# Performance work log

Hardware: AMD Instinct MI355X
Metric: run time of the kernel (lower is better)

Reference implementation:

```python
import jax, jax.numpy as jnp
import numpy as np

DIM = 128
WH, WW = 8, 8
N = WH * WW            # tokens per window = 64
H = 8                  # num_heads
HD = DIM // H          # head_dim = 16
SCALE = HD ** -0.5
B = 2                  # true batch
NW = 1024              # windows per image (256x256 / 8x8)
B_ = B * NW            # 2048 windows total
NFT = 2                # num_frame_type
TABLE = (2 * WH - 1) * (2 * WW - 1)  # 225


def _relative_position_index():
    coords = np.stack(np.meshgrid(np.arange(WH), np.arange(WW), indexing='ij'))  # (2, WH, WW)
    cf = coords.reshape(2, -1)                        # (2, N)
    rel = cf[:, :, None] - cf[:, None, :]             # (2, N, N)
    rel = rel.transpose(1, 2, 0).astype(np.int64)     # (N, N, 2)
    rel[..., 0] += WH - 1
    rel[..., 1] += WW - 1
    rel[..., 0] *= 2 * WW - 1
    return rel.sum(-1)                                # (N, N) in [0, 224]


def setup_inputs() -> dict:
    key = jax.random.key(0)
    ks = jax.random.split(key, 12)
    x = jax.random.normal(ks[0], (B_, N, DIM), dtype=jnp.float32)
    # 0 / -100 additive window mask (shifted-window pattern surrogate)
    mask = jnp.where(jax.random.uniform(ks[1], (NW, N, N)) > 0.9, -100.0, 0.0).astype(jnp.float32)
    frame_type = jax.random.uniform(ks[2], (B, NFT), dtype=jnp.float32)
    qkv_w = jax.random.normal(ks[3], (3 * DIM, DIM), dtype=jnp.float32) * 0.02
    qkv_b = jnp.zeros((3 * DIM,), dtype=jnp.float32)
    table = jax.random.normal(ks[4], (TABLE, H), dtype=jnp.float32) * 0.02
    proj_w = jax.random.normal(ks[5], (DIM, DIM), dtype=jnp.float32) * 0.02
    proj_b = jnp.zeros((DIM,), dtype=jnp.float32)
    aff_w1 = jax.random.normal(ks[6], (16, NFT), dtype=jnp.float32) * 0.1
    aff_b1 = jnp.zeros((16,), dtype=jnp.float32)
    aff_w2 = jax.random.normal(ks[7], (2 * DIM, 16), dtype=jnp.float32) * 0.1
    rel_index = jnp.asarray(_relative_position_index(), dtype=jnp.int32)
    return {"x": x, "mask": mask, "frame_type": frame_type,
            "qkv_w": qkv_w, "qkv_b": qkv_b, "table": table,
            "proj_w": proj_w, "proj_b": proj_b,
            "aff_w1": aff_w1, "aff_b1": aff_b1, "aff_w2": aff_w2,
            "rel_index": rel_index}


def reference(x, mask, frame_type, qkv_w, qkv_b, table, proj_w, proj_b,
              aff_w1, aff_b1, aff_w2, rel_index):
    # qkv projection: (B_, N, 3C) -> (3, B_, H, N, HD)
    qkv = (x @ qkv_w.T + qkv_b).reshape(B_, N, 3, H, HD).transpose(2, 0, 3, 1, 4)
    q, k, v = qkv[0], qkv[1], qkv[2]
    attn = jnp.einsum('bhnd,bhmd->bhnm', q * SCALE, k)          # (B_, H, N, N)
    rpb = table[rel_index].transpose(2, 0, 1)                    # (H, N, N)
    attn = attn + rpb[None]
    # add window mask: (B, NW, H, N, N)
    attn = attn.reshape(B_ // NW, NW, H, N, N) + mask[None, :, None]
    attn = jax.nn.softmax(attn.reshape(B_, H, N, N), axis=-1)
    # FA affine modulation of V
    hdn = jax.nn.sigmoid(frame_type @ aff_w1.T + aff_b1)         # (B, 16)
    ap = hdn @ aff_w2.T                                          # (B, 2C)
    scale_p, bias_p = jnp.split(ap, 2, axis=-1)                  # each (B, C)
    scale_p = jnp.repeat(scale_p, B_ // B, axis=0).reshape(B_, H, 1, HD)
    bias_p = jnp.repeat(bias_p, B_ // B, axis=0).reshape(B_, H, 1, HD)
    v = jax.nn.softplus(scale_p) * v + bias_p
    out = jnp.einsum('bhnm,bhmd->bhnd', attn, v)                 # (B_, H, N, HD)
    out = out.transpose(0, 2, 1, 3).reshape(B_, N, DIM)
    return out @ proj_w.T + proj_b
```

## Files before the change

### kernel.cpp

```cpp
#include <hip/hip_runtime.h>
#include <hip/hip_bf16.h>

#define NWIN 2048
#define OFF_AFF 0
#define OFF_RPB 512
#define OFF_WQ  33280
#define OFF_WP  82432

typedef __attribute__((ext_vector_type(8))) __bf16 bf16x8;
typedef __attribute__((ext_vector_type(4))) float floatx4;

__global__ __launch_bounds__(256) void prep_kernel(
    const float* __restrict__ frame_type, const float* __restrict__ qkv_w,
    const float* __restrict__ table, const float* __restrict__ proj_w,
    const float* __restrict__ aff_w1, const float* __restrict__ aff_b1,
    const float* __restrict__ aff_w2, const int* __restrict__ rel_index,
    float* __restrict__ ws)
{
  const int gid = blockIdx.x * 256 + threadIdx.x;
  if (gid < 98304) {
    int j = gid & 7, lane = (gid >> 3) & 63, kt = (gid >> 9) & 3, nt = gid >> 11;
    int n = nt * 16 + (lane & 15);
    int k = kt * 32 + (lane >> 4) * 8 + j;
    ((__bf16*)(ws + OFF_WQ))[gid] = (__bf16)qkv_w[n * 128 + k];
  }
  if (gid < 16384) {
    int j = gid & 7, lane = (gid >> 3) & 63, kt = (gid >> 9) & 3, nt = gid >> 11;
    int n = nt * 16 + (lane & 15);
    int k = kt * 32 + (lane >> 4) * 8 + j;
    ((__bf16*)(ws + OFF_WP))[gid] = (__bf16)proj_w[n * 128 + k];
  }
  if (gid < 32768) {
    int h = gid >> 12, ij = gid & 4095;
    ws[OFF_RPB + gid] = table[rel_index[ij] * 8 + h];
  }
  if (gid < 512) {
    int b = gid >> 8, c2 = gid & 255;
    float hd[16];
    #pragma unroll
    for (int j = 0; j < 16; ++j) {
      float t = frame_type[b*2+0]*aff_w1[j*2+0] + frame_type[b*2+1]*aff_w1[j*2+1] + aff_b1[j];
      hd[j] = 1.0f / (1.0f + expf(-t));
    }
    float ap = 0.f;
    #pragma unroll
    for (int j = 0; j < 16; ++j) ap += hd[j] * aff_w2[c2*16 + j];
    float r = (c2 < 128) ? ((ap > 20.f) ? ap : log1pf(expf(ap))) : ap;
    ws[OFF_AFF + gid] = r;
  }
}

__global__ __launch_bounds__(256, 2) void attn_kernel(
    const float* __restrict__ x, const float* __restrict__ mask,
    const float* __restrict__ qkv_b, const float* __restrict__ proj_b,
    const float* __restrict__ ws, float* __restrict__ out)
{
  __shared__ __attribute__((aligned(16))) __bf16 sQ [64 * 136];
  __shared__ __attribute__((aligned(16))) __bf16 sK [64 * 136];
  __shared__ __attribute__((aligned(16))) __bf16 sVT[128 * 72];
  __shared__ __attribute__((aligned(16))) __bf16 sP [64 * 72];
  __shared__ __attribute__((aligned(16))) __bf16 sAO[64 * 136];

  const int w    = blockIdx.x;
  const int b    = w >> 10;
  const int tid  = threadIdx.x;
  const int wv   = tid >> 6;
  const int lane = tid & 63;
  const int quad = lane >> 4;
  const int l15  = lane & 15;

  bf16x8 zf;
  #pragma unroll
  for (int i = 0; i < 8; ++i) zf[i] = (__bf16)0.0f;

  bf16x8 af[4][4];
  {
    const float* xw = x + (size_t)w * 8192;
    #pragma unroll
    for (int mt = 0; mt < 4; ++mt)
      #pragma unroll
      for (int kt = 0; kt < 4; ++kt) {
        const float* p = xw + (mt*16 + l15) * 128 + kt*32 + quad*8;
        float4 f0 = *(const float4*)p;
        float4 f1 = *(const float4*)(p + 4);
        bf16x8 v;
        v[0]=(__bf16)f0.x; v[1]=(__bf16)f0.y; v[2]=(__bf16)f0.z; v[3]=(__bf16)f0.w;
        v[4]=(__bf16)f1.x; v[5]=(__bf16)f1.y; v[6]=(__bf16)f1.z; v[7]=(__bf16)f1.w;
        af[mt][kt] = v;
      }
  }

  {
    const __bf16* wq = (const __bf16*)(ws + OFF_WQ);
    for (int t = 0; t < 6; ++t) {
      const int nt = wv + t * 4;
      bf16x8 bfr[4];
      #pragma unroll
      for (int kt = 0; kt < 4; ++kt)
        bfr[kt] = *(const bf16x8*)(wq + ((size_t)(nt*4 + kt) * 64 + lane) * 8);
      const float bias = qkv_b[nt*16 + l15];
      const int col = nt*16 + l15;
      #pragma unroll
      for (int mt = 0; mt < 4; ++mt) {
        floatx4 acc = {bias, bias, bias, bias};
        #pragma unroll
        for (int kt = 0; kt < 4; ++kt)
          acc = __builtin_amdgcn_mfma_f32_16x16x32_bf16(af[mt][kt], bfr[kt], acc, 0, 0, 0);
        const int rowb = mt*16 + quad*4;
        if (nt < 8) {
          #pragma unroll
          for (int r = 0; r < 4; ++r) sQ[(rowb + r)*136 + col] = (__bf16)acc[r];
        } else if (nt < 16) {
          const int c = col - 128;
          #pragma unroll
          for (int r = 0; r < 4; ++r) sK[(rowb + r)*136 + c] = (__bf16)acc[r];
        } else {
          const int c = col - 256;
          const float sp = ws[OFF_AFF + b*256 + c];
          const float bp = ws[OFF_AFF + b*256 + 128 + c];
          #pragma unroll
          for (int r = 0; r < 4; ++r) sVT[c*72 + rowb + r] = (__bf16)fmaf(sp, acc[r], bp);
        }
      }
    }
  }
  __syncthreads();

  const int row0 = wv * 16;
  const float* mrow = mask + (size_t)(w & 1023) * 4096;
  const float* rpb  = ws + OFF_RPB;

  for (int h = 0; h < 8; ++h) {
    bf16x8 qa = zf;
    if (quad < 2) qa = *(const bf16x8*)(&sQ[(row0 + l15)*136 + h*16 + quad*8]);
    floatx4 s[4];
    #pragma unroll
    for (int jt = 0; jt < 4; ++jt) {
      bf16x8 kb = zf;
      if (quad < 2) kb = *(const bf16x8*)(&sK[(jt*16 + l15)*136 + h*16 + quad*8]);
      floatx4 z = {0.f, 0.f, 0.f, 0.f};
      s[jt] = __builtin_amdgcn_mfma_f32_16x16x32_bf16(qa, kb, z, 0, 0, 0);
    }
    float ev[4][4], rmax[4], rsum[4];
    #pragma unroll
    for (int r = 0; r < 4; ++r) rmax[r] = -1e30f;
    #pragma unroll
    for (int jt = 0; jt < 4; ++jt)
      #pragma unroll
      for (int r = 0; r < 4; ++r) {
        const int rr = row0 + quad*4 + r, cc = jt*16 + l15;
        float v = fmaf(s[jt][r], 0.25f, rpb[h*4096 + rr*64 + cc] + mrow[rr*64 + cc]);
        ev[jt][r] = v;
        rmax[r] = fmaxf(rmax[r], v);
      }
    #pragma unroll
    for (int m = 1; m < 16; m <<= 1)
      #pragma unroll
      for (int r = 0; r < 4; ++r) rmax[r] = fmaxf(rmax[r], __shfl_xor(rmax[r], m, 64));
    #pragma unroll
    for (int r = 0; r < 4; ++r) rsum[r] = 0.f;
    #pragma unroll
    for (int jt = 0; jt < 4; ++jt)
      #pragma unroll
      for (int r = 0; r < 4; ++r) { ev[jt][r] = __expf(ev[jt][r] - rmax[r]); rsum[r] += ev[jt][r]; }
    #pragma unroll
    for (int m = 1; m < 16; m <<= 1)
      #pragma unroll
      for (int r = 0; r < 4; ++r) rsum[r] += __shfl_xor(rsum[r], m, 64);
    float inv[4];
    #pragma unroll
    for (int r = 0; r < 4; ++r) inv[r] = 1.0f / rsum[r];
    #pragma unroll
    for (int jt = 0; jt < 4; ++jt)
      #pragma unroll
      for (int r = 0; r < 4; ++r)
        sP[(row0 + quad*4 + r)*72 + jt*16 + l15] = (__bf16)(ev[jt][r] * inv[r]);
    floatx4 o = {0.f, 0.f, 0.f, 0.f};
    #pragma unroll
    for (int kt = 0; kt < 2; ++kt) {
      bf16x8 pa = *(const bf16x8*)(&sP [(row0 + l15)*72 + kt*32 + quad*8]);
      bf16x8 vb = *(const bf16x8*)(&sVT[(h*16 + l15)*72 + kt*32 + quad*8]);
      o = __builtin_amdgcn_mfma_f32_16x16x32_bf16(pa, vb, o, 0, 0, 0);
    }
    #pragma unroll
    for (int r = 0; r < 4; ++r)
      sAO[(row0 + quad*4 + r)*136 + h*16 + l15] = (__bf16)o[r];
  }

  {
    bf16x8 aof[4];
    #pragma unroll
    for (int kt = 0; kt < 4; ++kt)
      aof[kt] = *(const bf16x8*)(&sAO[(row0 + l15)*136 + kt*32 + quad*8]);
    const __bf16* wp = (const __bf16*)(ws + OFF_WP);
    float* ow = out + (size_t)w * 8192;
    for (int nt = 0; nt < 8; ++nt) {
      bf16x8 bfr[4];
      #pragma unroll
      for (int kt = 0; kt < 4; ++kt)
        bfr[kt] = *(const bf16x8*)(wp + ((size_t)(nt*4 + kt) * 64 + lane) * 8);
      const float bias = proj_b[nt*16 + l15];
      floatx4 acc = {bias, bias, bias, bias};
      #pragma unroll
      for (int kt = 0; kt < 4; ++kt)
        acc = __builtin_amdgcn_mfma_f32_16x16x32_bf16(aof[kt], bfr[kt], acc, 0, 0, 0);
      #pragma unroll
      for (int r = 0; r < 4; ++r)
        ow[(row0 + quad*4 + r)*128 + nt*16 + l15] = acc[r];
    }
  }
}

extern "C" void kernel_launch(void* const* d_in, const int* in_sizes, int n_in,
                              void* d_out, int out_size, void* d_ws, size_t ws_size,
                              hipStream_t stream)
{
  const float* x          = (const float*)d_in[0];
  const float* mask       = (const float*)d_in[1];
  const float* frame_type = (const float*)d_in[2];
  const float* qkv_w      = (const float*)d_in[3];
  const float* qkv_b      = (const float*)d_in[4];
  const float* table      = (const float*)d_in[5];
  const float* proj_w     = (const float*)d_in[6];
  const float* proj_b     = (const float*)d_in[7];
  const float* aff_w1     = (const float*)d_in[8];
  const float* aff_b1     = (const float*)d_in[9];
  const float* aff_w2     = (const float*)d_in[10];
  const int*   rel_index  = (const int*)d_in[11];
  float* ws   = (float*)d_ws;
  float* outp = (float*)d_out;

  prep_kernel<<<384, 256, 0, stream>>>(frame_type, qkv_w, table, proj_w,
                                       aff_w1, aff_b1, aff_w2, rel_index, ws);
  attn_kernel<<<NWIN, 256, 0, stream>>>(x, mask, qkv_b, proj_b, ws, outp);
}
```

Baseline: 224.8 us.

## Fuse output projection into per-head loop and simplify softmax with exp2

```diff
diff --git a/kernel.cpp b/kernel.cpp
--- a/kernel.cpp
+++ b/kernel.cpp
@@ -2,13 +2,23 @@
 #include <hip/hip_bf16.h>
 
 #define NWIN 2048
+#define LOG2E 1.44269504f
+#define QSCALE 0.36067376f
+
 #define OFF_AFF 0
 #define OFF_RPB 512
 #define OFF_WQ  33280
-#define OFF_WP  82432
+#define OFF_WP  57856
 
 typedef __attribute__((ext_vector_type(8))) __bf16 bf16x8;
 typedef __attribute__((ext_vector_type(4))) float floatx4;
+typedef __attribute__((ext_vector_type(4))) short short4v;
+
+#if __has_builtin(__builtin_amdgcn_exp2f)
+#define EXP2F __builtin_amdgcn_exp2f
+#else
+#define EXP2F exp2f
+#endif
 
 __global__ __launch_bounds__(256) void prep_kernel(
     const float* __restrict__ frame_type, const float* __restrict__ qkv_w,
@@ -18,21 +28,22 @@
     float* __restrict__ ws)
 {
   const int gid = blockIdx.x * 256 + threadIdx.x;
-  if (gid < 98304) {
+  if (gid < 49152) {
     int j = gid & 7, lane = (gid >> 3) & 63, kt = (gid >> 9) & 3, nt = gid >> 11;
     int n = nt * 16 + (lane & 15);
     int k = kt * 32 + (lane >> 4) * 8 + j;
     ((__bf16*)(ws + OFF_WQ))[gid] = (__bf16)qkv_w[n * 128 + k];
   }
   if (gid < 16384) {
-    int j = gid & 7, lane = (gid >> 3) & 63, kt = (gid >> 9) & 3, nt = gid >> 11;
+    int j = gid & 3, lane = (gid >> 2) & 63, nt = (gid >> 8) & 7, h = gid >> 11;
     int n = nt * 16 + (lane & 15);
-    int k = kt * 32 + (lane >> 4) * 8 + j;
+    int k = h * 16 + (lane >> 4) * 4 + j;
     ((__bf16*)(ws + OFF_WP))[gid] = (__bf16)proj_w[n * 128 + k];
   }
   if (gid < 32768) {
-    int h = gid >> 12, ij = gid & 4095;
-    ws[OFF_RPB + gid] = table[rel_index[ij] * 8 + h];
+    int h = gid >> 12, rem = gid & 4095, row = rem >> 6, col = rem & 63;
+    int dst = h * 4096 + row * 64 + (col & 15) * 4 + (col >> 4);
+    ws[OFF_RPB + dst] = table[rel_index[rem] * 8 + h] * LOG2E;
   }
   if (gid < 512) {
     int b = gid >> 8, c2 = gid & 255;
@@ -50,16 +61,14 @@
   }
 }
 
-__global__ __launch_bounds__(256, 2) void attn_kernel(
+__global__ __launch_bounds__(256, 3) void attn_kernel(
     const float* __restrict__ x, const float* __restrict__ mask,
     const float* __restrict__ qkv_b, const float* __restrict__ proj_b,
     const float* __restrict__ ws, float* __restrict__ out)
 {
-  __shared__ __attribute__((aligned(16))) __bf16 sQ [64 * 136];
+  __shared__ __attribute__((aligned(16))) __bf16 sQP[64 * 136];
   __shared__ __attribute__((aligned(16))) __bf16 sK [64 * 136];
   __shared__ __attribute__((aligned(16))) __bf16 sVT[128 * 72];
-  __shared__ __attribute__((aligned(16))) __bf16 sP [64 * 72];
-  __shared__ __attribute__((aligned(16))) __bf16 sAO[64 * 136];
 
   const int w    = blockIdx.x;
   const int b    = w >> 10;
@@ -68,10 +77,7 @@
   const int lane = tid & 63;
   const int quad = lane >> 4;
   const int l15  = lane & 15;
-
-  bf16x8 zf;
-  #pragma unroll
-  for (int i = 0; i < 8; ++i) zf[i] = (__bf16)0.0f;
+  const int row0 = wv * 16;
 
   bf16x8 af[4][4];
   {
@@ -109,7 +115,7 @@
         const int rowb = mt*16 + quad*4;
         if (nt < 8) {
           #pragma unroll
-          for (int r = 0; r < 4; ++r) sQ[(rowb + r)*136 + col] = (__bf16)acc[r];
+          for (int r = 0; r < 4; ++r) sQP[(rowb + r)*136 + col] = (__bf16)(acc[r] * QSCALE);
         } else if (nt < 16) {
           const int c = col - 128;
           #pragma unroll
@@ -126,88 +132,90 @@
   }
   __syncthreads();
 
-  const int row0 = wv * 16;
-  const float* mrow = mask + (size_t)(w & 1023) * 4096;
-  const float* rpb  = ws + OFF_RPB;
-
+  short4v qa[8];
+  #pragma unroll
+  for (int h = 0; h < 8; ++h)
+    qa[h] = *(const short4v*)(&sQP[(row0 + l15)*136 + h*16 + quad*4]);
+
+  __bf16* sP = sQP + wv * 2176;
+
+  float mv[4][4];
+  {
+    const float* mrow = mask + (size_t)(w & 1023) * 4096;
+    #pragma unroll
+    for (int jt = 0; jt < 4; ++jt)
+      #pragma unroll
+      for (int r = 0; r < 4; ++r)
+        mv[jt][r] = mrow[(row0 + quad*4 + r)*64 + jt*16 + l15] * LOG2E;
+  }
+  floatx4 pacc[8];
+  #pragma unroll
+  for (int nt = 0; nt < 8; ++nt) {
+    float pb = proj_b[nt*16 + l15];
+    pacc[nt] = (floatx4){pb, pb, pb, pb};
+  }
+
+  bf16x8 ones;
+  #pragma unroll
+  for (int i = 0; i < 8; ++i) ones[i] = (__bf16)1.0f;
+
+  const float* rpb = ws + OFF_RPB;
+  const __bf16* wp = (const __bf16*)(ws + OFF_WP);
+
+  #pragma unroll 1
   for (int h = 0; h < 8; ++h) {
-    bf16x8 qa = zf;
-    if (quad < 2) qa = *(const bf16x8*)(&sQ[(row0 + l15)*136 + h*16 + quad*8]);
+    floatx4 rq[4];
+    #pragma unroll
+    for (int r = 0; r < 4; ++r)
+      rq[r] = *(const floatx4*)(rpb + h*4096 + (row0 + quad*4 + r)*64 + l15*4);
+    short4v wpf[8];
+    #pragma unroll
+    for (int nt = 0; nt < 8; ++nt)
+      wpf[nt] = *(const short4v*)(wp + ((size_t)(h*8 + nt)*64 + lane)*4);
+
+    short4v kb[4];
+    #pragma unroll
+    for (int jt = 0; jt < 4; ++jt)
+      kb[jt] = *(const short4v*)(&sK[(jt*16 + l15)*136 + h*16 + quad*4]);
+
     floatx4 s[4];
     #pragma unroll
     for (int jt = 0; jt < 4; ++jt) {
-      bf16x8 kb = zf;
-      if (quad < 2) kb = *(const bf16x8*)(&sK[(jt*16 + l15)*136 + h*16 + quad*8]);
-      floatx4 z = {0.f, 0.f, 0.f, 0.f};
-      s[jt] = __builtin_amdgcn_mfma_f32_16x16x32_bf16(qa, kb, z, 0, 0, 0);
-    }
-    float ev[4][4], rmax[4], rsum[4];
-    #pragma unroll
-    for (int r = 0; r < 4; ++r) rmax[r] = -1e30f;
+      floatx4 ci;
+      #pragma unroll
+      for (int r = 0; r < 4; ++r) ci[r] = rq[r][jt] + mv[jt][r];
+      s[jt] = __builtin_amdgcn_mfma_f32_16x16x16bf16_1k(qa[h], kb[jt], ci, 0, 0, 0);
+    }
     #pragma unroll
     for (int jt = 0; jt < 4; ++jt)
       #pragma unroll
-      for (int r = 0; r < 4; ++r) {
-        const int rr = row0 + quad*4 + r, cc = jt*16 + l15;
-        float v = fmaf(s[jt][r], 0.25f, rpb[h*4096 + rr*64 + cc] + mrow[rr*64 + cc]);
-        ev[jt][r] = v;
-        rmax[r] = fmaxf(rmax[r], v);
-      }
-    #pragma unroll
-    for (int m = 1; m < 16; m <<= 1)
-      #pragma unroll
-      for (int r = 0; r < 4; ++r) rmax[r] = fmaxf(rmax[r], __shfl_xor(rmax[r], m, 64));
-    #pragma unroll
-    for (int r = 0; r < 4; ++r) rsum[r] = 0.f;
-    #pragma unroll
-    for (int jt = 0; jt < 4; ++jt)
-      #pragma unroll
-      for (int r = 0; r < 4; ++r) { ev[jt][r] = __expf(ev[jt][r] - rmax[r]); rsum[r] += ev[jt][r]; }
-    #pragma unroll
-    for (int m = 1; m < 16; m <<= 1)
-      #pragma unroll
-      for (int r = 0; r < 4; ++r) rsum[r] += __shfl_xor(rsum[r], m, 64);
-    float inv[4];
-    #pragma unroll
-    for (int r = 0; r < 4; ++r) inv[r] = 1.0f / rsum[r];
-    #pragma unroll
-    for (int jt = 0; jt < 4; ++jt)
-      #pragma unroll
       for (int r = 0; r < 4; ++r)
-        sP[(row0 + quad*4 + r)*72 + jt*16 + l15] = (__bf16)(ev[jt][r] * inv[r]);
-    floatx4 o = {0.f, 0.f, 0.f, 0.f};
+        sP[(quad*4 + r)*72 + jt*16 + l15] = (__bf16)EXP2F(s[jt][r]);
+
+    floatx4 o2 = {0.f,0.f,0.f,0.f}, s2 = {0.f,0.f,0.f,0.f};
     #pragma unroll
     for (int kt = 0; kt < 2; ++kt) {
-      bf16x8 pa = *(const bf16x8*)(&sP [(row0 + l15)*72 + kt*32 + quad*8]);
+      bf16x8 pa = *(const bf16x8*)(&sP[l15*72 + kt*32 + quad*8]);
       bf16x8 vb = *(const bf16x8*)(&sVT[(h*16 + l15)*72 + kt*32 + quad*8]);
-      o = __builtin_amdgcn_mfma_f32_16x16x32_bf16(pa, vb, o, 0, 0, 0);
-    }
-    #pragma unroll
-    for (int r = 0; r < 4; ++r)
-      sAO[(row0 + quad*4 + r)*136 + h*16 + l15] = (__bf16)o[r];
-  }
-
-  {
-    bf16x8 aof[4];
-    #pragma unroll
-    for (int kt = 0; kt < 4; ++kt)
-      aof[kt] = *(const bf16x8*)(&sAO[(row0 + l15)*136 + kt*32 + quad*8]);
-    const __bf16* wp = (const __bf16*)(ws + OFF_WP);
+      o2 = __builtin_amdgcn_mfma_f32_16x16x32_bf16(vb, pa, o2, 0, 0, 0);
+      s2 = __builtin_amdgcn_mfma_f32_16x16x32_bf16(ones, pa, s2, 0, 0, 0);
+    }
+    const float inv = 1.0f / s2[0];
+    union { short4v s; __bf16 hh[4]; } u;
+    #pragma unroll
+    for (int r = 0; r < 4; ++r) u.hh[r] = (__bf16)(o2[r] * inv);
+    #pragma unroll
+    for (int nt = 0; nt < 8; ++nt)
+      pacc[nt] = __builtin_amdgcn_mfma_f32_16x16x16bf16_1k(u.s, wpf[nt], pacc[nt], 0, 0, 0);
+  }
+
+  {
     float* ow = out + (size_t)w * 8192;
-    for (int nt = 0; nt < 8; ++nt) {
-      bf16x8 bfr[4];
-      #pragma unroll
-      for (int kt = 0; kt < 4; ++kt)
-        bfr[kt] = *(const bf16x8*)(wp + ((size_t)(nt*4 + kt) * 64 + lane) * 8);
-      const float bias = proj_b[nt*16 + l15];
-      floatx4 acc = {bias, bias, bias, bias};
-      #pragma unroll
-      for (int kt = 0; kt < 4; ++kt)
-        acc = __builtin_amdgcn_mfma_f32_16x16x32_bf16(aof[kt], bfr[kt], acc, 0, 0, 0);
+    #pragma unroll
+    for (int nt = 0; nt < 8; ++nt)
       #pragma unroll
       for (int r = 0; r < 4; ++r)
-        ow[(row0 + quad*4 + r)*128 + nt*16 + l15] = acc[r];
-    }
+        ow[(row0 + quad*4 + r)*128 + nt*16 + l15] = pacc[nt][r];
   }
 }
 
@@ -230,7 +238,7 @@
   float* ws   = (float*)d_ws;
   float* outp = (float*)d_out;
 
-  prep_kernel<<<384, 256, 0, stream>>>(frame_type, qkv_w, table, proj_w,
+  prep_kernel<<<192, 256, 0, stream>>>(frame_type, qkv_w, table, proj_w,
                                        aff_w1, aff_b1, aff_w2, rel_index, ws);
   attn_kernel<<<NWIN, 256, 0, stream>>>(x, mask, qkv_b, proj_b, ws, outp);
 }
```

Result: faster. 219.6 us (-2.3%).
